# Kernel optimization log

Hardware: AMD Instinct MI355X
Metric: run time of the kernel (lower is better)

The kernel has to match this reference:

```python
import jax, jax.numpy as jnp
import numpy as np

WIN = (2, 7, 7)          # 3D window size
EMBED = 192
HEADS = 6
HEAD_DIM = EMBED // HEADS  # 32
N = WIN[0] * WIN[1] * WIN[2]  # 98
TABLE = (2 * WIN[0] - 1) * (2 * WIN[1] - 1) * (2 * WIN[2] - 1)  # 507


def _relative_position_index():
    d, h, w = WIN
    coords = np.stack(np.meshgrid(np.arange(d), np.arange(h), np.arange(w), indexing='ij'))
    cf = coords.reshape(3, -1)                      # [3, N]
    rel = cf[:, :, None] - cf[:, None, :]           # [3, N, N]
    rel = rel.transpose(1, 2, 0).astype(np.int64)   # [N, N, 3]
    rel[..., 0] += d - 1
    rel[..., 1] += h - 1
    rel[..., 2] += w - 1
    rel[..., 0] *= (2 * h - 1) * (2 * w - 1)
    rel[..., 1] *= 2 * w - 1
    return rel.sum(-1)                              # [N, N] in [0, TABLE)


def setup_inputs() -> dict:
    key = jax.random.key(0)
    ks = jax.random.split(key, 8)
    B, nw = 2048, 64
    x = jax.random.normal(ks[0], (B, N, EMBED), dtype=jnp.float32)
    mask = jax.random.normal(ks[1], (nw, N, N), dtype=jnp.float32)
    s = EMBED ** -0.5
    qkv_w = jax.random.normal(ks[2], (3 * EMBED, EMBED), dtype=jnp.float32) * s
    qkv_b = jax.random.normal(ks[3], (3 * EMBED,), dtype=jnp.float32) * 0.02
    o_w = jax.random.normal(ks[4], (EMBED, EMBED), dtype=jnp.float32) * s
    o_b = jax.random.normal(ks[5], (EMBED,), dtype=jnp.float32) * 0.02
    bias_table = jax.random.normal(ks[6], (TABLE, HEADS), dtype=jnp.float32) * 0.02
    rel_index = jnp.asarray(_relative_position_index(), dtype=jnp.int32)
    return {"x": x, "mask": mask, "qkv_w": qkv_w, "qkv_b": qkv_b,
            "o_w": o_w, "o_b": o_b, "bias_table": bias_table,
            "rel_index": rel_index}


def reference(x, mask, qkv_w, qkv_b, o_w, o_b, bias_table, rel_index):
    B, n, C = x.shape
    scale = HEAD_DIM ** -0.5
    qkv = x @ qkv_w.T + qkv_b                            # [B, N, 3C]
    qkv = qkv.reshape(B, n, 3, HEADS, HEAD_DIM).transpose(2, 0, 3, 1, 4)
    q, k, v = qkv[0], qkv[1], qkv[2]                     # [B, H, N, hd]
    attn = jnp.einsum('bhqd,bhkd->bhqk', q, k) * scale   # [B, H, N, N]
    # gathered relative position bias: [N, N, H] -> [H, N, N]
    bias = bias_table[rel_index.reshape(-1)].reshape(n, n, HEADS).transpose(2, 0, 1)
    attn = attn + bias[None]
    nw = mask.shape[0]
    attn = attn.reshape(B // nw, nw, HEADS, n, n) + mask[None, :, None]
    attn = jax.nn.softmax(attn.reshape(B, HEADS, n, n), axis=-1)
    out = jnp.einsum('bhqk,bhkd->bhqd', attn, v)         # [B, H, N, hd]
    out = out.transpose(0, 2, 1, 3).reshape(B, n, C)
    return out @ o_w.T + o_b
```

## Files before the change

### kernel.cpp

```cpp
#include <hip/hip_runtime.h>
#include <hip/hip_bf16.h>


#define NB   2048
#define NN   98
#define CC   192
#define NH   6
#define HD   32
#define NWIN 64
#define MM   (NB * NN)
#define HEADBLK (NN * HD)
#define TILE_BYTES 24576

typedef _Float16 half8  __attribute__((ext_vector_type(8)));
typedef _Float16 half4  __attribute__((ext_vector_type(4)));
typedef float    f32x4  __attribute__((ext_vector_type(4)));

struct __attribute__((packed, aligned(4))) half8u { half8 v; };

__device__ __forceinline__ f32x4 mfma16(half8 a, half8 b, f32x4 c) {
    return __builtin_amdgcn_mfma_f32_16x16x32_f16(a, b, c, 0, 0, 0);
}

typedef __attribute__((address_space(3))) unsigned int       lds_uint;
typedef __attribute__((address_space(1))) const unsigned int g_uint;
__device__ __forceinline__ void async_copy16(void* lds, const void* g) {
    __builtin_amdgcn_global_load_lds((g_uint*)g, (lds_uint*)lds, 16, 0, 0);
}

#define WS_QKV   0ull
#define WS_AO    231211008ull
#define WS_W2    308281344ull
#define XH_BYTES 77070336ull

__global__ __launch_bounds__(256) void wa_k0_prep(
    const float* __restrict__ x,
    const float* __restrict__ o_w, const float* __restrict__ qkv_w,
    const float* __restrict__ bias_table, const int* __restrict__ rel_index,
    const float* __restrict__ mask,
    _Float16* __restrict__ w2, _Float16* __restrict__ wqh,
    float* __restrict__ bm, _Float16* __restrict__ xh)
{
    int t = blockIdx.x * 256 + threadIdx.x;
    if (t < CC * CC) {
        w2[t] = (_Float16)o_w[t];
    } else if (t < 4 * CC * CC) {
        int e = t - CC * CC;
        wqh[e] = (_Float16)qkv_w[e];
    }
    const size_t stride = (size_t)gridDim.x * 256;
    const size_t total_g = (size_t)MM * CC / 8;
    for (size_t g = t; g < total_g; g += stride) {
        const float* s = x + g * 8;
        float4 v0 = *(const float4*)s;
        float4 v1 = *(const float4*)(s + 4);
        half8 hv = { (_Float16)v0.x, (_Float16)v0.y, (_Float16)v0.z, (_Float16)v0.w,
                     (_Float16)v1.x, (_Float16)v1.y, (_Float16)v1.z, (_Float16)v1.w };
        *(half8*)(xh + g * 8) = hv;
    }
    const size_t bm_total = (size_t)NWIN * NH * NN * 128;
    for (size_t e = t; e < bm_total; e += stride) {
        int j   = (int)(e & 127);
        int row = (int)(e >> 7);
        int i   = row % NN;
        int wh  = row / NN;
        int hh  = wh % NH;
        int ww  = wh / NH;
        float v = -1.0e30f;
        if (j < NN)
            v = (bias_table[rel_index[i * NN + j] * NH + hh]
               + mask[((size_t)ww * NN + i) * NN + j]) * 1.4426950408889634f;
        bm[e] = v;
    }
}

__global__ __launch_bounds__(256, 3) void wa_k1_qkv(
    const _Float16* __restrict__ xh, const _Float16* __restrict__ wqh,
    const float* __restrict__ qkv_b, _Float16* __restrict__ qkv)
{
    const int id = blockIdx.x;
    const int c8 = id & 7;
    const int r  = id >> 3;
    const int nb = r % 9;
    const int chunk = c8 * 98 + r / 9;
    __shared__ __align__(128) _Float16 As[2][64 * 192];

    const int tid  = threadIdx.x;
    const int lane = tid & 63, wave = tid >> 6;
    const int l16  = lane & 15, quad = lane >> 4;

    int soff[6];
    #pragma unroll
    for (int i = 0; i < 6; ++i) {
        int off = i * 4096 + wave * 1024 + lane * 16;
        int row = off / 384;
        int col = off - row * 384;
        soff[i] = row * 384 + (col ^ ((row & 7) << 4));
    }

    half8 breg[6][4];
    const _Float16* bbase = wqh + (size_t)(nb * 64 + l16) * CC + quad * 8;
    #pragma unroll
    for (int kk = 0; kk < 6; ++kk)
        #pragma unroll
        for (int nt = 0; nt < 4; ++nt)
            breg[kk][nt] = *(const half8*)(bbase + nt * 16 * CC + kk * 32);

    float bias[4];
    #pragma unroll
    for (int nt = 0; nt < 4; ++nt) bias[nt] = qkv_b[nb * 64 + nt * 16 + l16];

    asm volatile("" ::: "memory");

    const int s = nb / 3;
    const int mb0 = chunk * 4;

    {
        const char* xb = (const char*)xh + (size_t)mb0 * TILE_BYTES;
        char* dst = (char*)As[0] + wave * 1024;
        #pragma unroll
        for (int i = 0; i < 6; ++i)
            async_copy16(dst + i * 4096, xb + soff[i]);
    }

    const int sx = (l16 & 7) << 4;
    const int rr = (wave * 16 + l16) * 384;
    const int cb = quad * 16;

    #pragma unroll
    for (int t = 0; t < 4; ++t) {
        if (t < 3) {
            const char* xb = (const char*)xh + (size_t)(mb0 + t + 1) * TILE_BYTES;
            char* dst = (char*)As[(t + 1) & 1] + wave * 1024;
            #pragma unroll
            for (int i = 0; i < 6; ++i)
                async_copy16(dst + i * 4096, xb + soff[i]);
            asm volatile("s_waitcnt vmcnt(6)" ::: "memory");
        } else {
            asm volatile("s_waitcnt vmcnt(0)" ::: "memory");
        }
        __builtin_amdgcn_s_barrier();
        asm volatile("" ::: "memory");

        const char* asb = (const char*)As[t & 1];
        f32x4 acc[4] = {};
        #pragma unroll
        for (int kk = 0; kk < 6; ++kk) {
            half8 a0 = *(const half8*)(asb + rr + ((cb + kk * 64) ^ sx));
            #pragma unroll
            for (int nt = 0; nt < 4; ++nt)
                acc[nt] = mfma16(a0, breg[kk][nt], acc[nt]);
        }

        const int mb = mb0 + t;
        int bArr[4], iArr[4];
        #pragma unroll
        for (int rq = 0; rq < 4; ++rq) {
            int m = mb * 64 + wave * 16 + quad * 4 + rq;
            int b_ = m / NN;
            bArr[rq] = b_;
            iArr[rq] = m - b_ * NN;
        }
        #pragma unroll
        for (int nt = 0; nt < 4; ++nt) {
            int j  = nb * 64 + nt * 16 + l16;
            int rm = j - s * CC;
            int hh = rm >> 5;
            int d  = rm & 31;
            #pragma unroll
            for (int rq = 0; rq < 4; ++rq) {
                _Float16 val = (_Float16)(acc[nt][rq] + bias[nt]);
                if (s == 2)
                    qkv[((size_t)(bArr[rq] * 3 + 2) * NH + hh) * HEADBLK + d * NN + iArr[rq]] = val;
                else
                    qkv[((size_t)(bArr[rq] * 3 + s) * NH + hh) * HEADBLK + iArr[rq] * HD + d] = val;
            }
        }
        asm volatile("" ::: "memory");
        __builtin_amdgcn_s_barrier();
        asm volatile("" ::: "memory");
    }
}

__global__ __launch_bounds__(448, 6) void wa_k2_attn(
    const _Float16* __restrict__ qkv, const float* __restrict__ bm,
    _Float16* __restrict__ ao)
{
    const int h = blockIdx.x;
    const int b = blockIdx.y;
    const int w = b & (NWIN - 1);
    const _Float16* qp = qkv + ((size_t)(b * 3 + 0) * NH + h) * HEADBLK;
    const _Float16* kp = qkv + ((size_t)(b * 3 + 1) * NH + h) * HEADBLK;
    const _Float16* vt = qkv + ((size_t)(b * 3 + 2) * NH + h) * HEADBLK;

    __shared__ __align__(16) _Float16 P[112 * 136];

    const int tid  = threadIdx.x;
    const int lane = tid & 63, wave = tid >> 6;
    const int l16  = lane & 15, quad = lane >> 4;

    const int qrow = wave * 16 + l16;
    const int qrc  = qrow < NN ? qrow : NN - 1;

    const float scale2 = 0.17677669529663687f * 1.4426950408889634f;

    half8 bq = *(const half8*)(qp + qrc * HD + quad * 8);
    const float* bmrow = bm + ((size_t)(w * NH + h) * NN + qrc) * 128;

    f32x4 s[7];
    #pragma unroll
    for (int jt = 0; jt < 7; ++jt) {
        half8 ak = *(const half8*)(kp + (jt * 16 + l16) * HD + quad * 8);
        f32x4 z = {};
        s[jt] = mfma16(ak, bq, z);
    }
    #pragma unroll
    for (int jt = 0; jt < 7; ++jt) {
        float4 bmv = *(const float4*)(bmrow + jt * 16 + quad * 4);
        s[jt][0] = fmaf(s[jt][0], scale2, bmv.x);
        s[jt][1] = fmaf(s[jt][1], scale2, bmv.y);
        s[jt][2] = fmaf(s[jt][2], scale2, bmv.z);
        s[jt][3] = fmaf(s[jt][3], scale2, bmv.w);
    }

    f32x4 vm = s[0];
    #pragma unroll
    for (int jt = 1; jt < 7; ++jt) {
        vm[0] = fmaxf(vm[0], s[jt][0]); vm[1] = fmaxf(vm[1], s[jt][1]);
        vm[2] = fmaxf(vm[2], s[jt][2]); vm[3] = fmaxf(vm[3], s[jt][3]);
    }
    float mx = fmaxf(fmaxf(vm[0], vm[1]), fmaxf(vm[2], vm[3]));
    mx = fmaxf(mx, __shfl_xor(mx, 16));
    mx = fmaxf(mx, __shfl_xor(mx, 32));

    f32x4 vs = {};
    #pragma unroll
    for (int jt = 0; jt < 7; ++jt) {
        #pragma unroll
        for (int rr = 0; rr < 4; ++rr) {
            float p = __builtin_amdgcn_exp2f(s[jt][rr] - mx);
            s[jt][rr] = p;
            vs[rr] += p;
        }
    }
    float sum = (vs[0] + vs[1]) + (vs[2] + vs[3]);
    sum += __shfl_xor(sum, 16);
    sum += __shfl_xor(sum, 32);
    float inv = __builtin_amdgcn_rcpf(sum);

    _Float16* prow = P + qrow * 136;
    #pragma unroll
    for (int jt = 0; jt < 7; ++jt) {
        half4 hv = { (_Float16)s[jt][0], (_Float16)s[jt][1],
                     (_Float16)s[jt][2], (_Float16)s[jt][3] };
        *(half4*)(prow + jt * 16 + quad * 4) = hv;
    }
    { half4 z4 = {}; *(half4*)(prow + 112 + quad * 4) = z4; }

    float invr[4];
    #pragma unroll
    for (int rr = 0; rr < 4; ++rr) invr[rr] = __shfl(inv, quad * 4 + rr);

    half8 pa[4];
    #pragma unroll
    for (int kc = 0; kc < 4; ++kc)
        pa[kc] = *(const half8*)(P + qrow * 136 + kc * 32 + quad * 8);

    #pragma unroll
    for (int nt = 0; nt < 2; ++nt) {
        f32x4 acc = {};
        #pragma unroll
        for (int kc = 0; kc < 4; ++kc) {
            half8 vb = ((const half8u*)(vt + (nt * 16 + l16) * NN + kc * 32 + quad * 8))->v;
            acc = mfma16(pa[kc], vb, acc);
        }
        #pragma unroll
        for (int rr = 0; rr < 4; ++rr) {
            int i = wave * 16 + quad * 4 + rr;
            if (i < NN)
                ao[((size_t)b * NN + i) * CC + h * HD + nt * 16 + l16] =
                    (_Float16)(acc[rr] * invr[rr]);
        }
    }
}

__global__ __launch_bounds__(256, 3) void wa_k3_proj(
    const _Float16* __restrict__ ao, const _Float16* __restrict__ w2,
    const float* __restrict__ o_b, float* __restrict__ out)
{
    const int id = blockIdx.x;
    const int c8 = id & 7;
    const int r  = id >> 3;
    const int nb = r % 3;
    const int chunk = c8 * 98 + r / 3;
    __shared__ __align__(128) _Float16 As[2][64 * 192];

    const int tid  = threadIdx.x;
    const int lane = tid & 63, wave = tid >> 6;
    const int l16  = lane & 15, quad = lane >> 4;

    int soff[6];
    #pragma unroll
    for (int i = 0; i < 6; ++i) {
        int off = i * 4096 + wave * 1024 + lane * 16;
        int row = off / 384;
        int col = off - row * 384;
        soff[i] = row * 384 + (col ^ ((row & 7) << 4));
    }

    half8 breg[6][4];
    const _Float16* bbase = w2 + (size_t)(nb * 64 + l16) * CC + quad * 8;
    #pragma unroll
    for (int kk = 0; kk < 6; ++kk)
        #pragma unroll
        for (int nt = 0; nt < 4; ++nt)
            breg[kk][nt] = *(const half8*)(bbase + nt * 16 * CC + kk * 32);

    float ob[4];
    #pragma unroll
    for (int nt = 0; nt < 4; ++nt) ob[nt] = o_b[nb * 64 + nt * 16 + l16];

    asm volatile("" ::: "memory");

    const int mb0 = chunk * 4;
    {
        const char* xb = (const char*)ao + (size_t)mb0 * TILE_BYTES;
        char* dst = (char*)As[0] + wave * 1024;
        #pragma unroll
        for (int i = 0; i < 6; ++i)
            async_copy16(dst + i * 4096, xb + soff[i]);
    }

    const int sx = (l16 & 7) << 4;
    const int rr = (wave * 16 + l16) * 384;
    const int cb = quad * 16;

    #pragma unroll
    for (int t = 0; t < 4; ++t) {
        if (t < 3) {
            const char* xb = (const char*)ao + (size_t)(mb0 + t + 1) * TILE_BYTES;
            char* dst = (char*)As[(t + 1) & 1] + wave * 1024;
            #pragma unroll
            for (int i = 0; i < 6; ++i)
                async_copy16(dst + i * 4096, xb + soff[i]);
            asm volatile("s_waitcnt vmcnt(6)" ::: "memory");
        } else {
            asm volatile("s_waitcnt vmcnt(0)" ::: "memory");
        }
        __builtin_amdgcn_s_barrier();
        asm volatile("" ::: "memory");

        const char* asb = (const char*)As[t & 1];
        f32x4 acc[4] = {};
        #pragma unroll
        for (int kk = 0; kk < 6; ++kk) {
            half8 a0 = *(const half8*)(asb + rr + ((cb + kk * 64) ^ sx));
            #pragma unroll
            for (int nt = 0; nt < 4; ++nt)
                acc[nt] = mfma16(a0, breg[kk][nt], acc[nt]);
        }

        const int mb = mb0 + t;
        #pragma unroll
        for (int nt = 0; nt < 4; ++nt) {
            int e = nb * 64 + nt * 16 + l16;
            #pragma unroll
            for (int rq = 0; rq < 4; ++rq) {
                int m = mb * 64 + wave * 16 + quad * 4 + rq;
                out[(size_t)m * CC + e] = acc[nt][rq] + ob[nt];
            }
        }
        asm volatile("" ::: "memory");
        __builtin_amdgcn_s_barrier();
        asm volatile("" ::: "memory");
    }
}

extern "C" void kernel_launch(void* const* d_in, const int* in_sizes, int n_in,
                              void* d_out, int out_size, void* d_ws, size_t ws_size,
                              hipStream_t stream)
{
    const float* x          = (const float*)d_in[0];
    const float* mask       = (const float*)d_in[1];
    const float* qkv_w      = (const float*)d_in[2];
    const float* qkv_b      = (const float*)d_in[3];
    const float* o_w        = (const float*)d_in[4];
    const float* o_b        = (const float*)d_in[5];
    const float* bias_table = (const float*)d_in[6];
    const int*   rel_index  = (const int*)d_in[7];

    char* ws = (char*)d_ws;
    _Float16* qkv = (_Float16*)(ws + WS_QKV);
    _Float16* ao  = (_Float16*)(ws + WS_AO);
    _Float16* wqh = (_Float16*)(ws + WS_AO);
    _Float16* w2  = (_Float16*)(ws + WS_W2);
    float*    out = (float*)d_out;
    _Float16* xh  = (_Float16*)d_out;
    float*    bm  = (float*)((char*)d_out + XH_BYTES);

    wa_k0_prep<<<2048, 256, 0, stream>>>(
        x, o_w, qkv_w, bias_table, rel_index, mask, w2, wqh, bm, xh);
    wa_k1_qkv<<<7056, 256, 0, stream>>>(xh, wqh, qkv_b, qkv);
    wa_k2_attn<<<dim3(NH, NB), 448, 0, stream>>>(qkv, bm, ao);
    wa_k3_proj<<<2352, 256, 0, stream>>>(ao, w2, o_b, out);
}
```

Baseline: 703.4 us.

## Split QKV output into QK and global V-transpose with vectorized stores and triple buffering

The QKV projection now writes Q and K into a per-batch packed buffer and V into a global transposed [head*dim, M] buffer. Swapping MFMA operands lets each lane emit contiguous half4 (and float4 in the output projection) stores instead of scattered scalar writes. Both GEMM kernels move to triple-buffered LDS with two tiles prefetched ahead. The QKV kernel also processes 8 tiles per block instead of 4. These changes lower occupancy via launch bounds and the larger LDS footprint. The attention kernel reads V with a large MM stride, which may hurt its load locality.

After: 681.6 us. 3.1% less time.

```diff
diff --git a/kernel.cpp b/kernel.cpp
--- a/kernel.cpp
+++ b/kernel.cpp
@@ -28,7 +28,8 @@
     __builtin_amdgcn_global_load_lds((g_uint*)g, (lds_uint*)lds, 16, 0, 0);
 }
 
-#define WS_QKV   0ull
+#define WS_QK    0ull
+#define WS_VT    154140672ull
 #define WS_AO    231211008ull
 #define WS_W2    308281344ull
 #define XH_BYTES 77070336ull
@@ -74,16 +75,17 @@
     }
 }
 
-__global__ __launch_bounds__(256, 3) void wa_k1_qkv(
+__global__ __launch_bounds__(256, 2) void wa_k1_qkv(
     const _Float16* __restrict__ xh, const _Float16* __restrict__ wqh,
-    const float* __restrict__ qkv_b, _Float16* __restrict__ qkv)
+    const float* __restrict__ qkv_b, _Float16* __restrict__ qk,
+    _Float16* __restrict__ vtg)
 {
     const int id = blockIdx.x;
     const int c8 = id & 7;
     const int r  = id >> 3;
     const int nb = r % 9;
-    const int chunk = c8 * 98 + r / 9;
-    __shared__ __align__(128) _Float16 As[2][64 * 192];
+    const int chunk = c8 * 49 + r / 9;
+    __shared__ __align__(128) _Float16 As[3][64 * 192];
 
     const int tid  = threadIdx.x;
     const int lane = tid & 63, wave = tid >> 6;
@@ -98,6 +100,9 @@
         soff[i] = row * 384 + (col ^ ((row & 7) << 4));
     }
 
+    const int s   = nb / 3;
+    const int nbr = nb - s * 3;
+
     half8 breg[6][4];
     const _Float16* bbase = wqh + (size_t)(nb * 64 + l16) * CC + quad * 8;
     #pragma unroll
@@ -106,92 +111,112 @@
         for (int nt = 0; nt < 4; ++nt)
             breg[kk][nt] = *(const half8*)(bbase + nt * 16 * CC + kk * 32);
 
-    float bias[4];
-    #pragma unroll
-    for (int nt = 0; nt < 4; ++nt) bias[nt] = qkv_b[nb * 64 + nt * 16 + l16];
+    float4 biasq[4];
+    float  biasv[4];
+    if (s == 2) {
+        #pragma unroll
+        for (int nt = 0; nt < 4; ++nt) biasv[nt] = qkv_b[nb * 64 + nt * 16 + l16];
+    } else {
+        #pragma unroll
+        for (int nt = 0; nt < 4; ++nt)
+            biasq[nt] = *(const float4*)(qkv_b + nb * 64 + nt * 16 + quad * 4);
+    }
 
     asm volatile("" ::: "memory");
 
-    const int s = nb / 3;
-    const int mb0 = chunk * 4;
-
-    {
-        const char* xb = (const char*)xh + (size_t)mb0 * TILE_BYTES;
-        char* dst = (char*)As[0] + wave * 1024;
+    const char* xb0 = (const char*)xh + (size_t)chunk * 8 * TILE_BYTES;
+    #pragma unroll
+    for (int p = 0; p < 2; ++p) {
+        char* dst = (char*)As[p] + wave * 1024;
+        const char* src = xb0 + (size_t)p * TILE_BYTES;
         #pragma unroll
         for (int i = 0; i < 6; ++i)
-            async_copy16(dst + i * 4096, xb + soff[i]);
-    }
-
-    const int sx = (l16 & 7) << 4;
-    const int rr = (wave * 16 + l16) * 384;
-    const int cb = quad * 16;
-
-    #pragma unroll
-    for (int t = 0; t < 4; ++t) {
-        if (t < 3) {
-            const char* xb = (const char*)xh + (size_t)(mb0 + t + 1) * TILE_BYTES;
-            char* dst = (char*)As[(t + 1) & 1] + wave * 1024;
+            async_copy16(dst + i * 4096, src + soff[i]);
+    }
+
+    const int sx   = (l16 & 7) << 4;
+    const int rowb = (wave * 16 + l16) * 384;
+    const int cb   = quad * 16;
+
+    #pragma unroll
+    for (int t = 0; t < 8; ++t) {
+        if (t < 6) {
+            char* dst = (char*)As[(t + 2) % 3] + wave * 1024;
+            const char* src = xb0 + (size_t)(t + 2) * TILE_BYTES;
             #pragma unroll
             for (int i = 0; i < 6; ++i)
-                async_copy16(dst + i * 4096, xb + soff[i]);
-            asm volatile("s_waitcnt vmcnt(6)" ::: "memory");
+                async_copy16(dst + i * 4096, src + soff[i]);
+        }
+        if (t == 0)      asm volatile("s_waitcnt vmcnt(12)" ::: "memory");
+        else if (t == 1) asm volatile("s_waitcnt vmcnt(16)" ::: "memory");
+        else if (t < 6)  asm volatile("s_waitcnt vmcnt(20)" ::: "memory");
+        else if (t == 6) asm volatile("s_waitcnt vmcnt(14)" ::: "memory");
+        else             asm volatile("s_waitcnt vmcnt(8)"  ::: "memory");
+        __builtin_amdgcn_s_barrier();
+        asm volatile("" ::: "memory");
+
+        const char* asb = (const char*)As[t % 3];
+        const int mb = chunk * 8 + t;
+        f32x4 acc[4] = {};
+
+        if (s == 2) {
+            #pragma unroll
+            for (int kk = 0; kk < 6; ++kk) {
+                half8 a0 = *(const half8*)(asb + rowb + ((cb + kk * 64) ^ sx));
+                #pragma unroll
+                for (int nt = 0; nt < 4; ++nt)
+                    acc[nt] = mfma16(a0, breg[kk][nt], acc[nt]);
+            }
+            const int m0v = mb * 64 + wave * 16 + quad * 4;
+            #pragma unroll
+            for (int nt = 0; nt < 4; ++nt) {
+                int rm = nbr * 64 + nt * 16 + l16;
+                int hh = rm >> 5, d = rm & 31;
+                half4 hv = { (_Float16)(acc[nt][0] + biasv[nt]),
+                             (_Float16)(acc[nt][1] + biasv[nt]),
+                             (_Float16)(acc[nt][2] + biasv[nt]),
+                             (_Float16)(acc[nt][3] + biasv[nt]) };
+                *(half4*)(vtg + (size_t)(hh * 32 + d) * MM + m0v) = hv;
+            }
         } else {
-            asm volatile("s_waitcnt vmcnt(0)" ::: "memory");
-        }
+            #pragma unroll
+            for (int kk = 0; kk < 6; ++kk) {
+                half8 a0 = *(const half8*)(asb + rowb + ((cb + kk * 64) ^ sx));
+                #pragma unroll
+                for (int nt = 0; nt < 4; ++nt)
+                    acc[nt] = mfma16(breg[kk][nt], a0, acc[nt]);
+            }
+            const int m  = mb * 64 + wave * 16 + l16;
+            const int b_ = (int)((unsigned)m / 98u);
+            const int i  = m - b_ * 98;
+            const size_t bsbase = (size_t)(b_ * 2 + s) * NH;
+            #pragma unroll
+            for (int nt = 0; nt < 4; ++nt) {
+                int rm = nbr * 64 + nt * 16 + quad * 4;
+                int hh = rm >> 5, d0 = rm & 31;
+                half4 hv = { (_Float16)(acc[nt][0] + biasq[nt].x),
+                             (_Float16)(acc[nt][1] + biasq[nt].y),
+                             (_Float16)(acc[nt][2] + biasq[nt].z),
+                             (_Float16)(acc[nt][3] + biasq[nt].w) };
+                *(half4*)(qk + (bsbase + hh) * HEADBLK + i * HD + d0) = hv;
+            }
+        }
+        asm volatile("" ::: "memory");
         __builtin_amdgcn_s_barrier();
         asm volatile("" ::: "memory");
-
-        const char* asb = (const char*)As[t & 1];
-        f32x4 acc[4] = {};
-        #pragma unroll
-        for (int kk = 0; kk < 6; ++kk) {
-            half8 a0 = *(const half8*)(asb + rr + ((cb + kk * 64) ^ sx));
-            #pragma unroll
-            for (int nt = 0; nt < 4; ++nt)
-                acc[nt] = mfma16(a0, breg[kk][nt], acc[nt]);
-        }
-
-        const int mb = mb0 + t;
-        int bArr[4], iArr[4];
-        #pragma unroll
-        for (int rq = 0; rq < 4; ++rq) {
-            int m = mb * 64 + wave * 16 + quad * 4 + rq;
-            int b_ = m / NN;
-            bArr[rq] = b_;
-            iArr[rq] = m - b_ * NN;
-        }
-        #pragma unroll
-        for (int nt = 0; nt < 4; ++nt) {
-            int j  = nb * 64 + nt * 16 + l16;
-            int rm = j - s * CC;
-            int hh = rm >> 5;
-            int d  = rm & 31;
-            #pragma unroll
-            for (int rq = 0; rq < 4; ++rq) {
-                _Float16 val = (_Float16)(acc[nt][rq] + bias[nt]);
-                if (s == 2)
-                    qkv[((size_t)(bArr[rq] * 3 + 2) * NH + hh) * HEADBLK + d * NN + iArr[rq]] = val;
-                else
-                    qkv[((size_t)(bArr[rq] * 3 + s) * NH + hh) * HEADBLK + iArr[rq] * HD + d] = val;
-            }
-        }
-        asm volatile("" ::: "memory");
-        __builtin_amdgcn_s_barrier();
-        asm volatile("" ::: "memory");
     }
 }
 
 __global__ __launch_bounds__(448, 6) void wa_k2_attn(
-    const _Float16* __restrict__ qkv, const float* __restrict__ bm,
-    _Float16* __restrict__ ao)
+    const _Float16* __restrict__ qk, const _Float16* __restrict__ vtg,
+    const float* __restrict__ bm, _Float16* __restrict__ ao)
 {
     const int h = blockIdx.x;
     const int b = blockIdx.y;
     const int w = b & (NWIN - 1);
-    const _Float16* qp = qkv + ((size_t)(b * 3 + 0) * NH + h) * HEADBLK;
-    const _Float16* kp = qkv + ((size_t)(b * 3 + 1) * NH + h) * HEADBLK;
-    const _Float16* vt = qkv + ((size_t)(b * 3 + 2) * NH + h) * HEADBLK;
+    const _Float16* qp = qk + ((size_t)(b * 2 + 0) * NH + h) * HEADBLK;
+    const _Float16* kp = qk + ((size_t)(b * 2 + 1) * NH + h) * HEADBLK;
+    const _Float16* vtp = vtg + (size_t)h * 32 * MM + (size_t)b * NN;
 
     __shared__ __align__(16) _Float16 P[112 * 136];
 
@@ -271,7 +296,8 @@
         f32x4 acc = {};
         #pragma unroll
         for (int kc = 0; kc < 4; ++kc) {
-            half8 vb = ((const half8u*)(vt + (nt * 16 + l16) * NN + kc * 32 + quad * 8))->v;
+            half8 vb = ((const half8u*)(vtp + (size_t)(nt * 16 + l16) * MM
+                                        + kc * 32 + quad * 8))->v;
             acc = mfma16(pa[kc], vb, acc);
         }
         #pragma unroll
@@ -284,7 +310,7 @@
     }
 }
 
-__global__ __launch_bounds__(256, 3) void wa_k3_proj(
+__global__ __launch_bounds__(256, 2) void wa_k3_proj(
     const _Float16* __restrict__ ao, const _Float16* __restrict__ w2,
     const float* __restrict__ o_b, float* __restrict__ out)
 {
@@ -293,7 +319,7 @@
     const int r  = id >> 3;
     const int nb = r % 3;
     const int chunk = c8 * 98 + r / 3;
-    __shared__ __align__(128) _Float16 As[2][64 * 192];
+    __shared__ __align__(128) _Float16 As[3][64 * 192];
 
     const int tid  = threadIdx.x;
     const int lane = tid & 63, wave = tid >> 6;
@@ -316,59 +342,61 @@
         for (int nt = 0; nt < 4; ++nt)
             breg[kk][nt] = *(const half8*)(bbase + nt * 16 * CC + kk * 32);
 
-    float ob[4];
-    #pragma unroll
-    for (int nt = 0; nt < 4; ++nt) ob[nt] = o_b[nb * 64 + nt * 16 + l16];
+    float4 ob4[4];
+    #pragma unroll
+    for (int nt = 0; nt < 4; ++nt)
+        ob4[nt] = *(const float4*)(o_b + nb * 64 + nt * 16 + quad * 4);
 
     asm volatile("" ::: "memory");
 
-    const int mb0 = chunk * 4;
-    {
-        const char* xb = (const char*)ao + (size_t)mb0 * TILE_BYTES;
-        char* dst = (char*)As[0] + wave * 1024;
+    const char* xb0 = (const char*)ao + (size_t)chunk * 4 * TILE_BYTES;
+    #pragma unroll
+    for (int p = 0; p < 2; ++p) {
+        char* dst = (char*)As[p] + wave * 1024;
+        const char* src = xb0 + (size_t)p * TILE_BYTES;
         #pragma unroll
         for (int i = 0; i < 6; ++i)
-            async_copy16(dst + i * 4096, xb + soff[i]);
-    }
-
-    const int sx = (l16 & 7) << 4;
-    const int rr = (wave * 16 + l16) * 384;
-    const int cb = quad * 16;
+            async_copy16(dst + i * 4096, src + soff[i]);
+    }
+
+    const int sx   = (l16 & 7) << 4;
+    const int rowb = (wave * 16 + l16) * 384;
+    const int cb   = quad * 16;
 
     #pragma unroll
     for (int t = 0; t < 4; ++t) {
-        if (t < 3) {
-            const char* xb = (const char*)ao + (size_t)(mb0 + t + 1) * TILE_BYTES;
-            char* dst = (char*)As[(t + 1) & 1] + wave * 1024;
+        if (t < 2) {
+            char* dst = (char*)As[(t + 2) % 3] + wave * 1024;
+            const char* src = xb0 + (size_t)(t + 2) * TILE_BYTES;
             #pragma unroll
             for (int i = 0; i < 6; ++i)
-                async_copy16(dst + i * 4096, xb + soff[i]);
-            asm volatile("s_waitcnt vmcnt(6)" ::: "memory");
-        } else {
-            asm volatile("s_waitcnt vmcnt(0)" ::: "memory");
-        }
+                async_copy16(dst + i * 4096, src + soff[i]);
+        }
+        if (t == 0)      asm volatile("s_waitcnt vmcnt(12)" ::: "memory");
+        else if (t == 1) asm volatile("s_waitcnt vmcnt(16)" ::: "memory");
+        else if (t == 2) asm volatile("s_waitcnt vmcnt(14)" ::: "memory");
+        else             asm volatile("s_waitcnt vmcnt(8)"  ::: "memory");
         __builtin_amdgcn_s_barrier();
         asm volatile("" ::: "memory");
 
-        const char* asb = (const char*)As[t & 1];
+        const char* asb = (const char*)As[t % 3];
+        const int mb = chunk * 4 + t;
         f32x4 acc[4] = {};
         #pragma unroll
         for (int kk = 0; kk < 6; ++kk) {
-            half8 a0 = *(const half8*)(asb + rr + ((cb + kk * 64) ^ sx));
+            half8 a0 = *(const half8*)(asb + rowb + ((cb + kk * 64) ^ sx));
             #pragma unroll
             for (int nt = 0; nt < 4; ++nt)
-                acc[nt] = mfma16(a0, breg[kk][nt], acc[nt]);
-        }
-
-        const int mb = mb0 + t;
+                acc[nt] = mfma16(breg[kk][nt], a0, acc[nt]);
+        }
+
+        const int m = mb * 64 + wave * 16 + l16;
+        float* orow = out + (size_t)m * CC + nb * 64 + quad * 4;
         #pragma unroll
         for (int nt = 0; nt < 4; ++nt) {
-            int e = nb * 64 + nt * 16 + l16;
-            #pragma unroll
-            for (int rq = 0; rq < 4; ++rq) {
-                int m = mb * 64 + wave * 16 + quad * 4 + rq;
-                out[(size_t)m * CC + e] = acc[nt][rq] + ob[nt];
-            }
+            float4 o = { acc[nt][0] + ob4[nt].x, acc[nt][1] + ob4[nt].y,
+                         acc[nt][2] + ob4[nt].z, acc[nt][3] + ob4[nt].w };
+            *(float4*)(orow + nt * 16) = o;
         }
         asm volatile("" ::: "memory");
         __builtin_amdgcn_s_barrier();
@@ -390,7 +418,8 @@
     const int*   rel_index  = (const int*)d_in[7];
 
     char* ws = (char*)d_ws;
-    _Float16* qkv = (_Float16*)(ws + WS_QKV);
+    _Float16* qk  = (_Float16*)(ws + WS_QK);
+    _Float16* vtg = (_Float16*)(ws + WS_VT);
     _Float16* ao  = (_Float16*)(ws + WS_AO);
     _Float16* wqh = (_Float16*)(ws + WS_AO);
     _Float16* w2  = (_Float16*)(ws + WS_W2);
@@ -400,7 +429,7 @@
 
     wa_k0_prep<<<2048, 256, 0, stream>>>(
         x, o_w, qkv_w, bias_table, rel_index, mask, w2, wqh, bm, xh);
-    wa_k1_qkv<<<7056, 256, 0, stream>>>(xh, wqh, qkv_b, qkv);
-    wa_k2_attn<<<dim3(NH, NB), 448, 0, stream>>>(qkv, bm, ao);
+    wa_k1_qkv<<<3528, 256, 0, stream>>>(xh, wqh, qkv_b, qk, vtg);
+    wa_k2_attn<<<dim3(NH, NB), 448, 0, stream>>>(qk, vtg, bm, ao);
     wa_k3_proj<<<2352, 256, 0, stream>>>(ao, w2, o_b, out);
 }
```
